# Kernel optimization log

Hardware: AMD Instinct MI355X
Metric: run time of the kernel (lower is better)

The kernel has to match this reference:

```python
import jax, jax.numpy as jnp
import numpy as np

B, L, D = 4, 2048, 256
MAX_NGRAM = 3
SLOTS = 64


def setup_inputs() -> dict:
    key = jax.random.key(0)
    k1, k2, k3 = jax.random.split(key, 3)
    x = jax.random.normal(k1, (B, L, D), dtype=jnp.float32)
    memory = jax.random.normal(k2, (SLOTS, MAX_NGRAM, D), dtype=jnp.float32)
    pos_bias = jax.random.normal(k3, (SLOTS, MAX_NGRAM), dtype=jnp.float32)
    return {"x": x, "memory": memory, "pos_bias": pos_bias}


def _extract_ngrams(x, max_ngram):
    # Left-pad with max_ngram-1 zero vectors, then take max_ngram shifted views.
    b, l, d = x.shape
    xpad = jnp.concatenate([jnp.zeros((b, max_ngram - 1, d), x.dtype), x], axis=1)
    # ngrams[b, l, n] = xpad[b, n + l]  -> (B, L, N, d)
    return jnp.stack([xpad[:, n:n + l] for n in range(max_ngram)], axis=2)


def reference(x, memory, pos_bias):
    slots, max_ngram, d = memory.shape
    ngrams = _extract_ngrams(x, max_ngram)                      # (B, L, N, d)
    # Contraction over d replaces the huge (B,L,M,N,d) broadcast-multiply.
    sims = jnp.einsum('blnd,mnd->blmn', ngrams, memory)         # (B, L, M, N)
    scores = sims + pos_bias[None, None]                        # (B, L, M, N)
    best = jnp.argmax(scores, axis=-1)                          # (B, L, M) int
    # selected[b,l,m] = memory[m, best[b,l,m]]  -> (B, L, M, d)
    selected = memory[jnp.arange(slots)[None, None, :], best]
    return selected.sum(axis=2)                                 # (B, L, d)
```

## Files before the change

### kernel.cpp

```cpp
#include <hip/hip_runtime.h>
#include <stdint.h>

#define LL   2048
#define DD   256
#define SLOTS 64
#define MN   192
#define PT   8192

typedef _Float16 half8 __attribute__((ext_vector_type(8)));
typedef float    f32x4 __attribute__((ext_vector_type(4)));

#define FRAG_ELEMS (MN * DD)

__global__ __launch_bounds__(256) void prep_kernel(
    const float* __restrict__ mem,
    _Float16* __restrict__ aS_h, _Float16* __restrict__ aS_l,
    _Float16* __restrict__ bG_h, _Float16* __restrict__ bG_l)
{
    const int e = blockIdx.x * 256 + threadIdx.x;
    const int mn = e >> 8;
    const int d  = e & 255;
    const float v = mem[e];
    const _Float16 h  = (_Float16)v;
    const _Float16 lo = (_Float16)(v - (float)h);

    {
        const int tm = mn >> 4, r = mn & 15;
        const int c = d >> 5, q = (d >> 3) & 3, j = d & 7;
        const int i1 = ((tm * 8 + c) * 64 + (q * 16 + r)) * 8 + j;
        aS_h[i1] = h; aS_l[i1] = lo;
    }
    {
        const int c2 = mn >> 5, q2 = (mn >> 3) & 3, j2 = mn & 7;
        const int td = d >> 4, n2 = d & 15;
        const int i2 = ((td * 6 + c2) * 64 + (q2 * 16 + n2)) * 8 + j2;
        bG_h[i2] = h; bG_l[i2] = lo;
    }
}

__global__ __launch_bounds__(256) void fused_kernel(
    const float* __restrict__ x, const float* __restrict__ bias,
    const _Float16* __restrict__ aS_h, const _Float16* __restrict__ aS_l,
    const _Float16* __restrict__ bG_h, const _Float16* __restrict__ bG_l,
    float* __restrict__ out)
{
    __shared__ _Float16 xfh[2 * 8 * 64 * 8];
    __shared__ _Float16 xfl[2 * 8 * 64 * 8];
    __shared__ float    scores[MN * 33];
    __shared__ float    biasS[MN];
    __shared__ unsigned int selS[16 * 8];

    const int p0   = blockIdx.x * 16;
    const int tid  = threadIdx.x;
    const int lane = tid & 63;
    const int w    = tid >> 6;

    if (tid < 128) selS[tid] = 0u;
    if (tid < MN)  biasS[tid] = bias[tid];
    {
        const int c  = tid & 7;
        const int rr = tid >> 3;
        int g = p0 - 2 + rr;
        g = g < 0 ? 0 : (g > PT - 1 ? PT - 1 : g);
        const float4* xr = (const float4*)(x + (size_t)g * DD + c * 32);
        const int pt = rr >> 4, lr = rr & 15;
#pragma unroll
        for (int q = 0; q < 4; ++q) {
            const float4 u = xr[q * 2];
            const float4 v = xr[q * 2 + 1];
            float f[8] = {u.x, u.y, u.z, u.w, v.x, v.y, v.z, v.w};
            half8 hi, lo;
#pragma unroll
            for (int j = 0; j < 8; ++j) {
                const _Float16 h = (_Float16)f[j];
                hi[j] = h;
                lo[j] = (_Float16)(f[j] - (float)h);
            }
            const int base = ((pt * 8 + c) * 64 + q * 16 + lr) * 8;
            *(half8*)(xfh + base) = hi;
            *(half8*)(xfl + base) = lo;
        }
    }
    __syncthreads();

    {
        f32x4 acc[3][2];
#pragma unroll
        for (int i = 0; i < 3; ++i)
#pragma unroll
            for (int p = 0; p < 2; ++p) acc[i][p] = (f32x4){0.f, 0.f, 0.f, 0.f};

#pragma unroll 2
        for (int c = 0; c < 8; ++c) {
            half8 ah[3], al[3], bh[2], bl[2];
#pragma unroll
            for (int i = 0; i < 3; ++i) {
                const int tm = w * 3 + i;
                const size_t off = (size_t)((tm * 8 + c) * 64 + lane) * 8;
                ah[i] = *(const half8*)(aS_h + off);
                al[i] = *(const half8*)(aS_l + off);
            }
#pragma unroll
            for (int p = 0; p < 2; ++p) {
                const int base = ((p * 8 + c) * 64 + lane) * 8;
                bh[p] = *(const half8*)(xfh + base);
                bl[p] = *(const half8*)(xfl + base);
            }
#pragma unroll
            for (int i = 0; i < 3; ++i)
#pragma unroll
                for (int p = 0; p < 2; ++p) {
                    acc[i][p] = __builtin_amdgcn_mfma_f32_16x16x32_f16(ah[i], bh[p], acc[i][p], 0, 0, 0);
                    acc[i][p] = __builtin_amdgcn_mfma_f32_16x16x32_f16(ah[i], bl[p], acc[i][p], 0, 0, 0);
                    acc[i][p] = __builtin_amdgcn_mfma_f32_16x16x32_f16(al[i], bh[p], acc[i][p], 0, 0, 0);
                }
        }

        const int q = lane >> 4, col = lane & 15;
#pragma unroll
        for (int i = 0; i < 3; ++i) {
            const int tm = w * 3 + i;
#pragma unroll
            for (int p = 0; p < 2; ++p) {
                const int wp = p * 16 + col;
#pragma unroll
                for (int r = 0; r < 4; ++r) {
                    const int mn = tm * 16 + q * 4 + r;
                    scores[mn * 33 + wp] = acc[i][p][r];
                }
            }
        }
    }
    __syncthreads();

#pragma unroll
    for (int it = 0; it < 4; ++it) {
        const int t2 = tid + it * 256;
        const int pl = t2 & 15;
        const int m  = t2 >> 4;
        const int p  = p0 + pl;
        const int l  = p & (LL - 1);
        const float v0 = ((l >= 2) ? scores[(3 * m + 0) * 33 + pl + 0] : 0.f) + biasS[3 * m + 0];
        const float v1 = ((l >= 1) ? scores[(3 * m + 1) * 33 + pl + 1] : 0.f) + biasS[3 * m + 1];
        const float v2 =              scores[(3 * m + 2) * 33 + pl + 2]       + biasS[3 * m + 2];
        int bn = 0; float bv = v0;
        if (v1 > bv) { bv = v1; bn = 1; }
        if (v2 > bv) { bv = v2; bn = 2; }
        const int mnb = 3 * m + bn;
        atomicOr(&selS[pl * 8 + (mnb >> 5)], 1u << (mnb & 31));
    }
    __syncthreads();

    {
        const int q  = lane >> 4, col = lane & 15;
        const int qb = q * 8;
        unsigned int sw[6];
#pragma unroll
        for (int c = 0; c < 6; ++c) sw[c] = selS[col * 8 + c];

        f32x4 acc2[4];
#pragma unroll
        for (int i = 0; i < 4; ++i) acc2[i] = (f32x4){0.f, 0.f, 0.f, 0.f};

        const _Float16 ONE = (_Float16)1.f, ZERO = (_Float16)0.f;
#pragma unroll
        for (int c = 0; c < 6; ++c) {
            half8 sel;
#pragma unroll
            for (int j = 0; j < 8; ++j)
                sel[j] = ((sw[c] >> (qb + j)) & 1u) ? ONE : ZERO;
#pragma unroll
            for (int i = 0; i < 4; ++i) {
                const int td = w * 4 + i;
                const size_t off = (size_t)((td * 6 + c) * 64 + lane) * 8;
                const half8 mh = *(const half8*)(bG_h + off);
                const half8 ml = *(const half8*)(bG_l + off);
                acc2[i] = __builtin_amdgcn_mfma_f32_16x16x32_f16(sel, mh, acc2[i], 0, 0, 0);
                acc2[i] = __builtin_amdgcn_mfma_f32_16x16x32_f16(sel, ml, acc2[i], 0, 0, 0);
            }
        }

#pragma unroll
        for (int i = 0; i < 4; ++i) {
            const int td = w * 4 + i;
#pragma unroll
            for (int r = 0; r < 4; ++r) {
                out[(size_t)(p0 + q * 4 + r) * DD + td * 16 + col] = acc2[i][r];
            }
        }
    }
}

extern "C" void kernel_launch(void* const* d_in, const int* in_sizes, int n_in,
                              void* d_out, int out_size, void* d_ws, size_t ws_size,
                              hipStream_t stream) {
    (void)in_sizes; (void)n_in; (void)out_size; (void)ws_size;
    const float* x    = (const float*)d_in[0];
    const float* mem  = (const float*)d_in[1];
    const float* bias = (const float*)d_in[2];
    float* out = (float*)d_out;

    _Float16* aS_h = (_Float16*)d_ws;
    _Float16* aS_l = aS_h + FRAG_ELEMS;
    _Float16* bG_h = aS_l + FRAG_ELEMS;
    _Float16* bG_l = bG_h + FRAG_ELEMS;

    prep_kernel<<<FRAG_ELEMS / 256, 256, 0, stream>>>(mem, aS_h, aS_l, bG_h, bG_l);
    fused_kernel<<<PT / 16, 256, 0, stream>>>(x, bias, aS_h, aS_l, bG_h, bG_l, out);
}
```

Before: 80.74 us.

## Split fused kernel into score-select and gather-sum kernels with larger gather tiles

Splits the single fused kernel in two. The first computes scores and argmax and writes per-position selection bitmasks to workspace. The second uses those bitmasks as one-hot MFMA operands against memory fragments, processing 32 positions per block so each memory fragment load feeds two MFMA tiles. This aims to halve the global fragment loads in the gather phase and lower register pressure in each kernel, at the cost of an extra launch and a small bitmask round trip through global memory.

```diff
diff --git a/kernel.cpp b/kernel.cpp
--- a/kernel.cpp
+++ b/kernel.cpp
@@ -38,17 +38,16 @@
     }
 }
 
-__global__ __launch_bounds__(256) void fused_kernel(
+__global__ __launch_bounds__(256) void score_sel_kernel(
     const float* __restrict__ x, const float* __restrict__ bias,
     const _Float16* __restrict__ aS_h, const _Float16* __restrict__ aS_l,
-    const _Float16* __restrict__ bG_h, const _Float16* __restrict__ bG_l,
-    float* __restrict__ out)
+    uint32_t* __restrict__ sel_out)
 {
     __shared__ _Float16 xfh[2 * 8 * 64 * 8];
     __shared__ _Float16 xfl[2 * 8 * 64 * 8];
     __shared__ float    scores[MN * 33];
     __shared__ float    biasS[MN];
-    __shared__ unsigned int selS[16 * 8];
+    __shared__ uint32_t selS[16 * 8];
 
     const int p0   = blockIdx.x * 16;
     const int tid  = threadIdx.x;
@@ -151,44 +150,75 @@
     }
     __syncthreads();
 
-    {
-        const int q  = lane >> 4, col = lane & 15;
-        const int qb = q * 8;
-        unsigned int sw[6];
-#pragma unroll
-        for (int c = 0; c < 6; ++c) sw[c] = selS[col * 8 + c];
-
-        f32x4 acc2[4];
-#pragma unroll
-        for (int i = 0; i < 4; ++i) acc2[i] = (f32x4){0.f, 0.f, 0.f, 0.f};
-
-        const _Float16 ONE = (_Float16)1.f, ZERO = (_Float16)0.f;
-#pragma unroll
-        for (int c = 0; c < 6; ++c) {
-            half8 sel;
+    if (tid < 96) {
+        const int pl = tid / 6, c = tid % 6;
+        sel_out[p0 * 6 + tid] = selS[pl * 8 + c];
+    }
+}
+
+__global__ __launch_bounds__(256) void select_kernel(
+    const uint32_t* __restrict__ sel_in,
+    const _Float16* __restrict__ bG_h, const _Float16* __restrict__ bG_l,
+    float* __restrict__ out)
+{
+    __shared__ uint32_t selL[32 * 6];
+
+    const int p0   = blockIdx.x * 32;
+    const int tid  = threadIdx.x;
+    const int lane = tid & 63;
+    const int w    = tid >> 6;
+
+    if (tid < 192) selL[tid] = sel_in[p0 * 6 + tid];
+    __syncthreads();
+
+    const int q  = lane >> 4, col = lane & 15;
+    const int qb = q * 8;
+
+    uint32_t sw[2][6];
+#pragma unroll
+    for (int pt = 0; pt < 2; ++pt)
+#pragma unroll
+        for (int c = 0; c < 6; ++c) sw[pt][c] = selL[(pt * 16 + col) * 6 + c];
+
+    f32x4 acc[2][4];
+#pragma unroll
+    for (int pt = 0; pt < 2; ++pt)
+#pragma unroll
+        for (int i = 0; i < 4; ++i) acc[pt][i] = (f32x4){0.f, 0.f, 0.f, 0.f};
+
+    const _Float16 ONE = (_Float16)1.f, ZERO = (_Float16)0.f;
+#pragma unroll 2
+    for (int c = 0; c < 6; ++c) {
+        half8 sel[2];
+#pragma unroll
+        for (int pt = 0; pt < 2; ++pt)
 #pragma unroll
             for (int j = 0; j < 8; ++j)
-                sel[j] = ((sw[c] >> (qb + j)) & 1u) ? ONE : ZERO;
-#pragma unroll
-            for (int i = 0; i < 4; ++i) {
-                const int td = w * 4 + i;
-                const size_t off = (size_t)((td * 6 + c) * 64 + lane) * 8;
-                const half8 mh = *(const half8*)(bG_h + off);
-                const half8 ml = *(const half8*)(bG_l + off);
-                acc2[i] = __builtin_amdgcn_mfma_f32_16x16x32_f16(sel, mh, acc2[i], 0, 0, 0);
-                acc2[i] = __builtin_amdgcn_mfma_f32_16x16x32_f16(sel, ml, acc2[i], 0, 0, 0);
-            }
-        }
-
+                sel[pt][j] = ((sw[pt][c] >> (qb + j)) & 1u) ? ONE : ZERO;
 #pragma unroll
         for (int i = 0; i < 4; ++i) {
             const int td = w * 4 + i;
+            const size_t off = (size_t)((td * 6 + c) * 64 + lane) * 8;
+            const half8 mh = *(const half8*)(bG_h + off);
+            const half8 ml = *(const half8*)(bG_l + off);
+#pragma unroll
+            for (int pt = 0; pt < 2; ++pt) {
+                acc[pt][i] = __builtin_amdgcn_mfma_f32_16x16x32_f16(sel[pt], mh, acc[pt][i], 0, 0, 0);
+                acc[pt][i] = __builtin_amdgcn_mfma_f32_16x16x32_f16(sel[pt], ml, acc[pt][i], 0, 0, 0);
+            }
+        }
+    }
+
+#pragma unroll
+    for (int pt = 0; pt < 2; ++pt)
+#pragma unroll
+        for (int i = 0; i < 4; ++i) {
+            const int td = w * 4 + i;
 #pragma unroll
             for (int r = 0; r < 4; ++r) {
-                out[(size_t)(p0 + q * 4 + r) * DD + td * 16 + col] = acc2[i][r];
-            }
-        }
-    }
+                out[(size_t)(p0 + pt * 16 + q * 4 + r) * DD + td * 16 + col] = acc[pt][i][r];
+            }
+        }
 }
 
 extern "C" void kernel_launch(void* const* d_in, const int* in_sizes, int n_in,
@@ -204,7 +234,9 @@
     _Float16* aS_l = aS_h + FRAG_ELEMS;
     _Float16* bG_h = aS_l + FRAG_ELEMS;
     _Float16* bG_l = bG_h + FRAG_ELEMS;
+    uint32_t* sel  = (uint32_t*)(bG_l + FRAG_ELEMS);
 
     prep_kernel<<<FRAG_ELEMS / 256, 256, 0, stream>>>(mem, aS_h, aS_l, bG_h, bG_l);
-    fused_kernel<<<PT / 16, 256, 0, stream>>>(x, bias, aS_h, aS_l, bG_h, bG_l, out);
-}
+    score_sel_kernel<<<PT / 16, 256, 0, stream>>>(x, bias, aS_h, aS_l, sel);
+    select_kernel<<<PT / 32, 256, 0, stream>>>(sel, bG_h, bG_l, out);
+}
```

New measurement: 90.48 us. 1.12x slower.

## Double-buffer MFMA fragment loads, drop low-half memory in gather, shrink score tile

Applied to the files above, without the earlier changes.

Fragment loads in both GEMM loops are now register double-buffered: the next chunk's A/B (or memory) fragments are loaded while the current MFMAs run. The first gather fragments are prefetched before the argmax barrier. The gather GEMM now uses only the fp16 high part of memory, so the low-part buffer, its prep writes and half of the gather MFMAs go away. The scores shared array shrinks to the 18 columns that are actually read. The trade-off is reduced output precision (fp16-rounded memory values summed over 64 slots) and higher register pressure from the buffers.

```diff
diff --git a/kernel.cpp b/kernel.cpp
--- a/kernel.cpp
+++ b/kernel.cpp
@@ -15,7 +15,7 @@
 __global__ __launch_bounds__(256) void prep_kernel(
     const float* __restrict__ mem,
     _Float16* __restrict__ aS_h, _Float16* __restrict__ aS_l,
-    _Float16* __restrict__ bG_h, _Float16* __restrict__ bG_l)
+    _Float16* __restrict__ bG_h)
 {
     const int e = blockIdx.x * 256 + threadIdx.x;
     const int mn = e >> 8;
@@ -34,29 +34,40 @@
         const int c2 = mn >> 5, q2 = (mn >> 3) & 3, j2 = mn & 7;
         const int td = d >> 4, n2 = d & 15;
         const int i2 = ((td * 6 + c2) * 64 + (q2 * 16 + n2)) * 8 + j2;
-        bG_h[i2] = h; bG_l[i2] = lo;
+        bG_h[i2] = h;
     }
 }
 
 __global__ __launch_bounds__(256) void fused_kernel(
     const float* __restrict__ x, const float* __restrict__ bias,
     const _Float16* __restrict__ aS_h, const _Float16* __restrict__ aS_l,
-    const _Float16* __restrict__ bG_h, const _Float16* __restrict__ bG_l,
+    const _Float16* __restrict__ bG_h,
     float* __restrict__ out)
 {
     __shared__ _Float16 xfh[2 * 8 * 64 * 8];
     __shared__ _Float16 xfl[2 * 8 * 64 * 8];
-    __shared__ float    scores[MN * 33];
+    __shared__ float    scores[MN * 18];
     __shared__ float    biasS[MN];
-    __shared__ unsigned int selS[16 * 8];
+    __shared__ uint32_t selS[16 * 8];
 
     const int p0   = blockIdx.x * 16;
     const int tid  = threadIdx.x;
     const int lane = tid & 63;
     const int w    = tid >> 6;
+    const int q    = lane >> 4, col = lane & 15;
+
+    half8 ah[2][3], al[2][3];
+#pragma unroll
+    for (int i = 0; i < 3; ++i) {
+        const int tm = w * 3 + i;
+        const size_t off = (size_t)((tm * 8 + 0) * 64 + lane) * 8;
+        ah[0][i] = *(const half8*)(aS_h + off);
+        al[0][i] = *(const half8*)(aS_l + off);
+    }
 
     if (tid < 128) selS[tid] = 0u;
     if (tid < MN)  biasS[tid] = bias[tid];
+
     {
         const int c  = tid & 7;
         const int rr = tid >> 3;
@@ -65,9 +76,9 @@
         const float4* xr = (const float4*)(x + (size_t)g * DD + c * 32);
         const int pt = rr >> 4, lr = rr & 15;
 #pragma unroll
-        for (int q = 0; q < 4; ++q) {
-            const float4 u = xr[q * 2];
-            const float4 v = xr[q * 2 + 1];
+        for (int qq = 0; qq < 4; ++qq) {
+            const float4 u = xr[qq * 2];
+            const float4 v = xr[qq * 2 + 1];
             float f[8] = {u.x, u.y, u.z, u.w, v.x, v.y, v.z, v.w};
             half8 hi, lo;
 #pragma unroll
@@ -76,7 +87,7 @@
                 hi[j] = h;
                 lo[j] = (_Float16)(f[j] - (float)h);
             }
-            const int base = ((pt * 8 + c) * 64 + q * 16 + lr) * 8;
+            const int base = ((pt * 8 + c) * 64 + qq * 16 + lr) * 8;
             *(half8*)(xfh + base) = hi;
             *(half8*)(xfl + base) = lo;
         }
@@ -90,46 +101,63 @@
 #pragma unroll
             for (int p = 0; p < 2; ++p) acc[i][p] = (f32x4){0.f, 0.f, 0.f, 0.f};
 
-#pragma unroll 2
+        half8 bh[2][2], bl[2][2];
+#pragma unroll
+        for (int p = 0; p < 2; ++p) {
+            const int base = ((p * 8 + 0) * 64 + lane) * 8;
+            bh[0][p] = *(const half8*)(xfh + base);
+            bl[0][p] = *(const half8*)(xfl + base);
+        }
+
+#pragma unroll
         for (int c = 0; c < 8; ++c) {
-            half8 ah[3], al[3], bh[2], bl[2];
-#pragma unroll
-            for (int i = 0; i < 3; ++i) {
-                const int tm = w * 3 + i;
-                const size_t off = (size_t)((tm * 8 + c) * 64 + lane) * 8;
-                ah[i] = *(const half8*)(aS_h + off);
-                al[i] = *(const half8*)(aS_l + off);
-            }
-#pragma unroll
-            for (int p = 0; p < 2; ++p) {
-                const int base = ((p * 8 + c) * 64 + lane) * 8;
-                bh[p] = *(const half8*)(xfh + base);
-                bl[p] = *(const half8*)(xfl + base);
+            const int cur = c & 1, nxt = cur ^ 1;
+            if (c < 7) {
+#pragma unroll
+                for (int i = 0; i < 3; ++i) {
+                    const int tm = w * 3 + i;
+                    const size_t off = (size_t)((tm * 8 + c + 1) * 64 + lane) * 8;
+                    ah[nxt][i] = *(const half8*)(aS_h + off);
+                    al[nxt][i] = *(const half8*)(aS_l + off);
+                }
+#pragma unroll
+                for (int p = 0; p < 2; ++p) {
+                    const int base = ((p * 8 + c + 1) * 64 + lane) * 8;
+                    bh[nxt][p] = *(const half8*)(xfh + base);
+                    bl[nxt][p] = *(const half8*)(xfl + base);
+                }
             }
 #pragma unroll
             for (int i = 0; i < 3; ++i)
 #pragma unroll
                 for (int p = 0; p < 2; ++p) {
-                    acc[i][p] = __builtin_amdgcn_mfma_f32_16x16x32_f16(ah[i], bh[p], acc[i][p], 0, 0, 0);
-                    acc[i][p] = __builtin_amdgcn_mfma_f32_16x16x32_f16(ah[i], bl[p], acc[i][p], 0, 0, 0);
-                    acc[i][p] = __builtin_amdgcn_mfma_f32_16x16x32_f16(al[i], bh[p], acc[i][p], 0, 0, 0);
-                }
-        }
-
-        const int q = lane >> 4, col = lane & 15;
+                    acc[i][p] = __builtin_amdgcn_mfma_f32_16x16x32_f16(ah[cur][i], bh[cur][p], acc[i][p], 0, 0, 0);
+                    acc[i][p] = __builtin_amdgcn_mfma_f32_16x16x32_f16(ah[cur][i], bl[cur][p], acc[i][p], 0, 0, 0);
+                    acc[i][p] = __builtin_amdgcn_mfma_f32_16x16x32_f16(al[cur][i], bh[cur][p], acc[i][p], 0, 0, 0);
+                }
+        }
+
 #pragma unroll
         for (int i = 0; i < 3; ++i) {
             const int tm = w * 3 + i;
 #pragma unroll
             for (int p = 0; p < 2; ++p) {
                 const int wp = p * 16 + col;
-#pragma unroll
-                for (int r = 0; r < 4; ++r) {
-                    const int mn = tm * 16 + q * 4 + r;
-                    scores[mn * 33 + wp] = acc[i][p][r];
-                }
-            }
-        }
+                if (wp < 18) {
+#pragma unroll
+                    for (int r = 0; r < 4; ++r)
+                        scores[(tm * 16 + q * 4 + r) * 18 + wp] = acc[i][p][r];
+                }
+            }
+        }
+    }
+
+    half8 mg[2][4];
+#pragma unroll
+    for (int i = 0; i < 4; ++i) {
+        const int td = w * 4 + i;
+        const size_t off = (size_t)((td * 6 + 0) * 64 + lane) * 8;
+        mg[0][i] = *(const half8*)(bG_h + off);
     }
     __syncthreads();
 
@@ -140,9 +168,9 @@
         const int m  = t2 >> 4;
         const int p  = p0 + pl;
         const int l  = p & (LL - 1);
-        const float v0 = ((l >= 2) ? scores[(3 * m + 0) * 33 + pl + 0] : 0.f) + biasS[3 * m + 0];
-        const float v1 = ((l >= 1) ? scores[(3 * m + 1) * 33 + pl + 1] : 0.f) + biasS[3 * m + 1];
-        const float v2 =              scores[(3 * m + 2) * 33 + pl + 2]       + biasS[3 * m + 2];
+        const float v0 = ((l >= 2) ? scores[(3 * m + 0) * 18 + pl + 0] : 0.f) + biasS[3 * m + 0];
+        const float v1 = ((l >= 1) ? scores[(3 * m + 1) * 18 + pl + 1] : 0.f) + biasS[3 * m + 1];
+        const float v2 =              scores[(3 * m + 2) * 18 + pl + 2]       + biasS[3 * m + 2];
         int bn = 0; float bv = v0;
         if (v1 > bv) { bv = v1; bn = 1; }
         if (v2 > bv) { bv = v2; bn = 2; }
@@ -152,41 +180,42 @@
     __syncthreads();
 
     {
-        const int q  = lane >> 4, col = lane & 15;
+        uint32_t sw[6];
+#pragma unroll
+        for (int c = 0; c < 6; ++c) sw[c] = selS[col * 8 + c];
+
+        f32x4 acc2[4];
+#pragma unroll
+        for (int i = 0; i < 4; ++i) acc2[i] = (f32x4){0.f, 0.f, 0.f, 0.f};
+
+        const _Float16 ONE = (_Float16)1.f, ZERO = (_Float16)0.f;
         const int qb = q * 8;
-        unsigned int sw[6];
-#pragma unroll
-        for (int c = 0; c < 6; ++c) sw[c] = selS[col * 8 + c];
-
-        f32x4 acc2[4];
-#pragma unroll
-        for (int i = 0; i < 4; ++i) acc2[i] = (f32x4){0.f, 0.f, 0.f, 0.f};
-
-        const _Float16 ONE = (_Float16)1.f, ZERO = (_Float16)0.f;
 #pragma unroll
         for (int c = 0; c < 6; ++c) {
+            const int cur = c & 1, nxt = cur ^ 1;
+            if (c < 5) {
+#pragma unroll
+                for (int i = 0; i < 4; ++i) {
+                    const int td = w * 4 + i;
+                    const size_t off = (size_t)((td * 6 + c + 1) * 64 + lane) * 8;
+                    mg[nxt][i] = *(const half8*)(bG_h + off);
+                }
+            }
             half8 sel;
 #pragma unroll
             for (int j = 0; j < 8; ++j)
                 sel[j] = ((sw[c] >> (qb + j)) & 1u) ? ONE : ZERO;
 #pragma unroll
-            for (int i = 0; i < 4; ++i) {
-                const int td = w * 4 + i;
-                const size_t off = (size_t)((td * 6 + c) * 64 + lane) * 8;
-                const half8 mh = *(const half8*)(bG_h + off);
-                const half8 ml = *(const half8*)(bG_l + off);
-                acc2[i] = __builtin_amdgcn_mfma_f32_16x16x32_f16(sel, mh, acc2[i], 0, 0, 0);
-                acc2[i] = __builtin_amdgcn_mfma_f32_16x16x32_f16(sel, ml, acc2[i], 0, 0, 0);
-            }
+            for (int i = 0; i < 4; ++i)
+                acc2[i] = __builtin_amdgcn_mfma_f32_16x16x32_f16(sel, mg[cur][i], acc2[i], 0, 0, 0);
         }
 
 #pragma unroll
         for (int i = 0; i < 4; ++i) {
             const int td = w * 4 + i;
 #pragma unroll
-            for (int r = 0; r < 4; ++r) {
+            for (int r = 0; r < 4; ++r)
                 out[(size_t)(p0 + q * 4 + r) * DD + td * 16 + col] = acc2[i][r];
-            }
         }
     }
 }
@@ -203,8 +232,7 @@
     _Float16* aS_h = (_Float16*)d_ws;
     _Float16* aS_l = aS_h + FRAG_ELEMS;
     _Float16* bG_h = aS_l + FRAG_ELEMS;
-    _Float16* bG_l = bG_h + FRAG_ELEMS;
-
-    prep_kernel<<<FRAG_ELEMS / 256, 256, 0, stream>>>(mem, aS_h, aS_l, bG_h, bG_l);
-    fused_kernel<<<PT / 16, 256, 0, stream>>>(x, bias, aS_h, aS_l, bG_h, bG_l, out);
+
+    prep_kernel<<<FRAG_ELEMS / 256, 256, 0, stream>>>(mem, aS_h, aS_l, bG_h);
+    fused_kernel<<<PT / 16, 256, 0, stream>>>(x, bias, aS_h, aS_l, bG_h, out);
 }
```

New measurement: 76.25 us (median of 2 runs). 1.06x faster.
